# Kernel optimization log

Hardware: AMD Instinct MI355X
Metric: run time of the kernel (lower is better)

## Reference

```python
import jax, jax.numpy as jnp
import numpy as np

K = 3      # kernel size
PAD = 1    # padding
EPS = 1e-5 # BatchNorm eps


def conv3x3(x, w, b):
    out = jax.lax.conv_general_dilated(
        x, w, window_strides=(1, 1), padding=((PAD, PAD), (PAD, PAD)),
        dimension_numbers=('NCHW', 'OIHW', 'NCHW'))
    return out + b[None, :, None, None]


def bilinear_gather(x, py, px):
    # x: [B,C,H,W]; py,px: [B,K2,H,W] fractional sample coords (zero pad OOB)
    B, C, H, W = x.shape
    y0 = jnp.floor(py)
    x0 = jnp.floor(px)
    wy1 = py - y0
    wx1 = px - x0
    xf = x.reshape(B, C, H * W)

    def corner(yc, xc, wgt):
        valid = (yc >= 0) & (yc <= H - 1) & (xc >= 0) & (xc <= W - 1)
        yi = jnp.clip(yc, 0, H - 1).astype(jnp.int32)
        xi = jnp.clip(xc, 0, W - 1).astype(jnp.int32)
        idx = yi * W + xi                      # [B,K2,H,W]
        g = jax.vmap(lambda img, ix: jnp.take(img, ix, axis=1))(xf, idx.reshape(B, -1))
        g = g.reshape(B, C, idx.shape[1], H, W)  # [B,C,K2,H,W]
        return g * (wgt * valid)[:, None]

    return (corner(y0,     x0,     (1 - wy1) * (1 - wx1))
            + corner(y0,     x0 + 1, (1 - wy1) * wx1)
            + corner(y0 + 1, x0,     wy1 * (1 - wx1))
            + corner(y0 + 1, x0 + 1, wy1 * wx1))


def deform_conv_bn_relu(x, offset_w, offset_b, mod_w, mod_b, weight, bias, gamma, beta):
    B, Ci, H, W = x.shape
    Co = weight.shape[0]
    K2 = K * K
    # offset / modulator branches (dense 3x3 convs)
    off = conv3x3(x, offset_w, offset_b)                  # [B,2*K2,H,W]
    mask = 2.0 * jax.nn.sigmoid(conv3x3(x, mod_w, mod_b))  # [B,K2,H,W]
    off = off.reshape(B, K2, 2, H, W)
    dy, dx = off[:, :, 0], off[:, :, 1]
    # base sampling grid per kernel tap
    ii, jj = jnp.meshgrid(jnp.arange(K), jnp.arange(K), indexing='ij')
    ky = ii.reshape(-1).astype(x.dtype)                    # [K2]
    kx = jj.reshape(-1).astype(x.dtype)
    hh = jnp.arange(H, dtype=x.dtype)
    ww = jnp.arange(W, dtype=x.dtype)
    py = hh[None, None, :, None] - PAD + ky[None, :, None, None] + dy  # [B,K2,H,W]
    px = ww[None, None, None, :] - PAD + kx[None, :, None, None] + dx
    sampled = bilinear_gather(x, py, px)                   # [B,Ci,K2,H,W]
    sampled = sampled * mask[:, None]                      # modulated (DCNv2)
    out = jnp.einsum('bckhw,ock->bohw', sampled, weight.reshape(Co, Ci, K2))
    out = out + bias[None, :, None, None]
    # BatchNorm (batch statistics) + ReLU
    mu = out.mean(axis=(0, 2, 3), keepdims=True)
    var = out.var(axis=(0, 2, 3), keepdims=True)
    y = (out - mu) * jax.lax.rsqrt(var + EPS) * gamma[None, :, None, None] + beta[None, :, None, None]
    return jax.nn.relu(y)


def setup_inputs() -> dict:
    key = jax.random.key(0)
    ks = jax.random.split(key, 4)
    B, Ci, Co, H, W = 8, 256, 256, 64, 64
    x = jax.random.normal(ks[0], (B, Ci, H, W), jnp.float32)
    offset_w = jax.random.normal(ks[1], (2 * K * K, Ci, K, K), jnp.float32) * 0.01
    offset_b = jnp.zeros((2 * K * K,), jnp.float32)
    mod_w = jax.random.normal(ks[2], (K * K, Ci, K, K), jnp.float32) * 0.01
    mod_b = jnp.zeros((K * K,), jnp.float32)
    weight = jax.random.normal(ks[3], (Co, Ci, K, K), jnp.float32) * (1.0 / np.sqrt(Ci * K * K))
    bias = jnp.zeros((Co,), jnp.float32)
    gamma = jnp.ones((Co,), jnp.float32)
    beta = jnp.zeros((Co,), jnp.float32)
    return {"x": x, "offset_w": offset_w, "offset_b": offset_b,
            "mod_w": mod_w, "mod_b": mod_b, "weight": weight, "bias": bias,
            "gamma": gamma, "beta": beta}


def reference(x, offset_w, offset_b, mod_w, mod_b, weight, bias, gamma, beta):
    return deform_conv_bn_relu(x, offset_w, offset_b, mod_w, mod_b, weight, bias, gamma, beta)
```

## Files before the change

### kernel.cpp

```cpp
#include <hip/hip_runtime.h>
#include <math.h>

#define CI 256
#define CO 256
#define HWN 4096

typedef short bf16x8 __attribute__((ext_vector_type(8)));
typedef float f32x4 __attribute__((ext_vector_type(4)));

__device__ inline unsigned pk2(float a, float b) {
  unsigned ua = __float_as_uint(a), ub = __float_as_uint(b);
  ua += 0x7fff + ((ua >> 16) & 1);
  ub += 0x7fff + ((ub >> 16) & 1);
  return (ua >> 16) | (ub & 0xffff0000u);
}

#define PIPE_BARRIER()                                    \
  do {                                                    \
    __builtin_amdgcn_sched_barrier(0);                    \
    asm volatile("s_waitcnt lgkmcnt(0)" ::: "memory");    \
    __builtin_amdgcn_s_barrier();                         \
    __builtin_amdgcn_sched_barrier(0);                    \
  } while (0)

__global__ __launch_bounds__(256) void k_prep(
    const float* __restrict__ x, const float* __restrict__ wgt,
    const float* __restrict__ ow, const float* __restrict__ mw,
    unsigned short* __restrict__ wT, unsigned short* __restrict__ wTo,
    unsigned short* __restrict__ xhp) {
  const int bid = blockIdx.x, tid = threadIdx.x;
  if (bid < 4096) {
    int i = bid * 256 + tid;
    const float4* xf = (const float4*)x;
    float4 a = xf[2 * i], b = xf[2 * i + 1];
    ((uint4*)xhp)[i] = make_uint4(pk2(a.x, a.y), pk2(a.z, a.w), pk2(b.x, b.y),
                                  pk2(b.z, b.w));
  } else if (bid < 4352) {
    int o = bid - 4096, c = tid;
    const float* wp = wgt + o * 2304 + c * 9;
    float v[9];
#pragma unroll
    for (int t = 0; t < 9; ++t) v[t] = wp[t];
#pragma unroll
    for (int t = 0; t < 9; ++t) {
      unsigned u = __float_as_uint(v[t]);
      u += 0x7fff + ((u >> 16) & 1);
      wT[(t << 16) + (o << 8) + c] = (unsigned short)(u >> 16);
    }
  } else {
    int o = bid - 4352, c = tid;
    float v[9];
    if (o < 18) {
      const float* wp = ow + o * 2304 + c * 9;
#pragma unroll
      for (int t = 0; t < 9; ++t) v[t] = wp[t];
    } else if (o < 27) {
      const float* wp = mw + (o - 18) * 2304 + c * 9;
#pragma unroll
      for (int t = 0; t < 9; ++t) v[t] = wp[t];
    } else {
#pragma unroll
      for (int t = 0; t < 9; ++t) v[t] = 0.f;
    }
#pragma unroll
    for (int t = 0; t < 9; ++t) {
      unsigned u = __float_as_uint(v[t]);
      u += 0x7fff + ((u >> 16) & 1);
      wTo[(t << 13) + (o << 8) + c] = (unsigned short)(u >> 16);
    }
  }
}

__global__ __launch_bounds__(512, 4) void k_fused2(
    const unsigned short* __restrict__ xh, const unsigned short* __restrict__ wT,
    const unsigned short* __restrict__ wTo, const float* __restrict__ ob,
    const float* __restrict__ mb, float* __restrict__ out,
    float* __restrict__ psum, float* __restrict__ psq) {
  __shared__ __align__(16) char smem[47872];
  uint2* s_cw = (uint2*)smem;
  ushort2* s_ci = (ushort2*)(smem + 4608);
  char* sA = smem + 6912;
  char* sB = smem + 15104;
  float* tr = (float*)(smem + 6912);
  char* sA0 = smem + 6912;
  char* sA1 = smem + 15104;
  char* sB0 = smem + 23296;
  char* sB1 = smem + 27392;
  float* s_red = (float*)(smem + 6912);
  float* s_off = (float*)(smem + 31488);

  const int tid = threadIdx.x;
  const int mblk = blockIdx.x;
  const int b = mblk >> 6, h = mblk & 63;
  const int lane = tid & 63;
  const int wv = tid >> 6;
  const char* xbh = (const char*)(xh + (size_t)b * (CI * HWN));

  {
    const int grp = wv >> 2;
    const int lw = wv & 3;
    const int gtid = tid & 255;
    const int px = lane;
    char* sAg = grp ? sA1 : sA0;
    char* sBg = grp ? sB1 : sB0;
    f32x4 pacc[2];
    pacc[0] = (f32x4){0.f, 0.f, 0.f, 0.f};
    pacc[1] = (f32x4){0.f, 0.f, 0.f, 0.f};

    unsigned rxu[16];
    float cwA, cwB;
    {
      int y0 = h - 1, x0 = px - 1;
      float w = (((unsigned)y0 < 64u) && ((unsigned)x0 < 64u)) ? 1.f : 0.f;
      int y0c = min(max(y0, 0), 63);
      int xp = min(max(x0, 0), 62);
      int s0 = min(max(x0, 0), 63) - xp;
      cwA = s0 ? 0.f : w;
      cwB = s0 ? w : 0.f;
      int ci = y0c * 64 + xp;
#pragma unroll
      for (int g2 = 0; g2 < 2; ++g2) {
        int g = lw + (g2 << 2);
#pragma unroll
        for (int j = 0; j < 8; ++j) {
          int c = ((grp << 1) << 6) + (g << 3) + j;
          __builtin_memcpy(&rxu[(g2 << 3) + j], xbh + (((c << 12) + ci) << 1),
                           4);
        }
      }
    }

#pragma unroll 1
    for (int t = 0; t < 18; ++t) {
      const int cqi = t / 9;
      const int tap = t - cqi * 9;
      const int cq = (grp << 1) + cqi;
#pragma unroll
      for (int g2 = 0; g2 < 2; ++g2) {
        unsigned pkv[4];
#pragma unroll
        for (int j2 = 0; j2 < 4; ++j2) {
          unsigned d0 = rxu[(g2 << 3) + (j2 << 1)];
          unsigned d1 = rxu[(g2 << 3) + (j2 << 1) + 1];
          float v0 = cwA * __uint_as_float(d0 << 16);
          v0 = fmaf(cwB, __uint_as_float(d0 & 0xffff0000u), v0);
          float v1 = cwA * __uint_as_float(d1 << 16);
          v1 = fmaf(cwB, __uint_as_float(d1 & 0xffff0000u), v1);
          pkv[j2] = pk2(v0, v1);
        }
        int g = lw + (g2 << 2);
        *(uint4*)(sAg + (px << 7) + ((g ^ (px & 7)) << 4)) =
            make_uint4(pkv[0], pkv[1], pkv[2], pkv[3]);
      }
      {
        int o = gtid >> 3, seg = gtid & 7;
        uint4 v = *(const uint4*)(wTo + (tap << 13) + (o << 8) + (cq << 6) +
                                  (seg << 3));
        *(uint4*)(sBg + (o << 7) + ((seg ^ (o & 7)) << 4)) = v;
      }
      {
        const int tn = t < 17 ? t + 1 : 17;
        const int cqni = tn / 9;
        const int tapn = tn - cqni * 9;
        const int cqn = (grp << 1) + cqni;
        int ky = tapn / 3, kx = tapn - 3 * ky;
        int y0 = h - 1 + ky, x0 = px - 1 + kx;
        float w = (((unsigned)y0 < 64u) && ((unsigned)x0 < 64u)) ? 1.f : 0.f;
        int y0c = min(max(y0, 0), 63);
        int xp = min(max(x0, 0), 62);
        int s0 = min(max(x0, 0), 63) - xp;
        float cwAn = s0 ? 0.f : w;
        float cwBn = s0 ? w : 0.f;
        int ci = y0c * 64 + xp;
#pragma unroll
        for (int g2 = 0; g2 < 2; ++g2) {
          int g = lw + (g2 << 2);
#pragma unroll
          for (int j = 0; j < 8; ++j) {
            int c = (cqn << 6) + (g << 3) + j;
            __builtin_memcpy(&rxu[(g2 << 3) + j],
                             xbh + (((c << 12) + ci) << 1), 4);
          }
        }
        cwA = cwAn;
        cwB = cwBn;
      }
      PIPE_BARRIER();
#pragma unroll
      for (int ks = 0; ks < 2; ++ks) {
        int arow = (lw << 4) + (lane & 15);
        int aslt = ((ks << 2) + (lane >> 4)) ^ (arow & 7);
        bf16x8 af = *(bf16x8*)(sAg + (arow << 7) + (aslt << 4));
#pragma unroll
        for (int nf = 0; nf < 2; ++nf) {
          int brow = (nf << 4) + (lane & 15);
          int bslt = ((ks << 2) + (lane >> 4)) ^ (brow & 7);
          bf16x8 bfr = *(bf16x8*)(sBg + (brow << 7) + (bslt << 4));
          pacc[nf] = __builtin_amdgcn_mfma_f32_16x16x32_bf16(af, bfr, pacc[nf],
                                                             0, 0, 0);
        }
      }
      PIPE_BARRIER();
    }
    if (grp == 1) {
#pragma unroll
      for (int nf = 0; nf < 2; ++nf)
#pragma unroll
        for (int r = 0; r < 4; ++r) s_red[gtid * 8 + nf * 4 + r] = pacc[nf][r];
    }
    __syncthreads();
    if (grp == 0) {
#pragma unroll
      for (int nf = 0; nf < 2; ++nf) {
#pragma unroll
        for (int r = 0; r < 4; ++r)
          pacc[nf][r] += s_red[gtid * 8 + nf * 4 + r];
        int o = (nf << 4) + (lane & 15);
        int px0 = (lw << 4) + ((lane >> 4) << 2);
        if (o < 18) {
          float bo = ob[o];
          *(float4*)(s_off + o * 64 + px0) =
              make_float4(pacc[nf][0] + bo, pacc[nf][1] + bo, pacc[nf][2] + bo,
                          pacc[nf][3] + bo);
        } else if (o < 27) {
          float bm = mb[o - 18];
          float4 v;
          v.x = 2.f / (1.f + expf(-(pacc[nf][0] + bm)));
          v.y = 2.f / (1.f + expf(-(pacc[nf][1] + bm)));
          v.z = 2.f / (1.f + expf(-(pacc[nf][2] + bm)));
          v.w = 2.f / (1.f + expf(-(pacc[nf][3] + bm)));
          *(float4*)(s_off + o * 64 + px0) = v;
        }
      }
    }
    __syncthreads();
  }

  for (int i = tid; i < 576; i += 512) {
    int k = i >> 6, pxi = i & 63;
    float dy = s_off[(2 * k) * 64 + pxi];
    float dx = s_off[(2 * k + 1) * 64 + pxi];
    float m = s_off[(18 + k) * 64 + pxi];
    float py = (float)(h - 1 + k / 3) + dy;
    float pxf = (float)(pxi - 1 + k % 3) + dx;
    float y0f = floorf(py), x0f = floorf(pxf);
    float wy = py - y0f, wx = pxf - x0f;
    int y0 = (int)y0f, x0 = (int)x0f;
    int y1 = y0 + 1, x1 = x0 + 1;
    float w00 = (1.f - wy) * (1.f - wx) * m;
    float w01 = (1.f - wy) * wx * m;
    float w10 = wy * (1.f - wx) * m;
    float w11 = wy * wx * m;
    bool vy0 = ((unsigned)y0 < 64u), vy1 = ((unsigned)y1 < 64u);
    bool vx0 = ((unsigned)x0 < 64u), vx1 = ((unsigned)x1 < 64u);
    if (!(vy0 && vx0)) w00 = 0.f;
    if (!(vy0 && vx1)) w01 = 0.f;
    if (!(vy1 && vx0)) w10 = 0.f;
    if (!(vy1 && vx1)) w11 = 0.f;
    int y0c = min(max(y0, 0), 63), y1c = min(max(y1, 0), 63);
    int x0c = min(max(x0, 0), 63), x1c = min(max(x1, 0), 63);
    int xp = min(max(x0, 0), 62);
    int s0 = x0c - xp, s1 = x1c - xp;
    float a0 = (s0 ? 0.f : w00) + (s1 ? 0.f : w01);
    float b0 = (s0 ? w00 : 0.f) + (s1 ? w01 : 0.f);
    float a1 = (s0 ? 0.f : w10) + (s1 ? 0.f : w11);
    float b1 = (s0 ? w10 : 0.f) + (s1 ? w11 : 0.f);
    s_cw[i] = make_uint2(pk2(a0, b0), pk2(a1, b1));
    s_ci[i] = make_ushort2((unsigned short)(y0c * 64 + xp),
                           (unsigned short)(y1c * 64 + xp));
  }
  __syncthreads();

  f32x4 acc[4][2];
#pragma unroll
  for (int mf = 0; mf < 4; ++mf)
#pragma unroll
    for (int nf = 0; nf < 2; ++nf) acc[mf][nf] = (f32x4){0.f, 0.f, 0.f, 0.f};

  const int aslot = (lane << 7) + ((wv ^ (lane & 7)) << 4);

  unsigned rxu[16];
  float4 cwC;
  {
    uint2 p = s_cw[lane];
    cwC.x = __uint_as_float(p.x << 16);
    cwC.y = __uint_as_float(p.x & 0xffff0000u);
    cwC.z = __uint_as_float(p.y << 16);
    cwC.w = __uint_as_float(p.y & 0xffff0000u);
    ushort2 ci0 = s_ci[lane];
    const char* xcn = xbh + (((wv << 3) * HWN) << 1);
#pragma unroll
    for (int s = 0; s < 8; ++s) {
      const char* xc = xcn + ((s * HWN) << 1);
      __builtin_memcpy(&rxu[2 * s + 0], xc + ((int)ci0.x << 1), 4);
      __builtin_memcpy(&rxu[2 * s + 1], xc + ((int)ci0.y << 1), 4);
    }
  }

#pragma unroll 1
  for (int t = 0; t < 36; ++t) {
    const int cq = t / 9;
    const int tap = t - cq * 9;
    {
      unsigned pkv[4];
#pragma unroll
      for (int j2 = 0; j2 < 4; ++j2) {
        float vv[2];
#pragma unroll
        for (int u = 0; u < 2; ++u) {
          unsigned d0 = rxu[4 * j2 + 2 * u], d1 = rxu[4 * j2 + 2 * u + 1];
          float v = cwC.x * __uint_as_float(d0 << 16);
          v = fmaf(cwC.y, __uint_as_float(d0 & 0xffff0000u), v);
          v = fmaf(cwC.z, __uint_as_float(d1 << 16), v);
          vv[u] = fmaf(cwC.w, __uint_as_float(d1 & 0xffff0000u), v);
        }
        pkv[j2] = pk2(vv[0], vv[1]);
      }
      *(uint4*)(sA + aslot) = make_uint4(pkv[0], pkv[1], pkv[2], pkv[3]);
    }
    {
      const unsigned short* wp = wT + (tap << 16) + (cq << 6);
#pragma unroll
      for (int r = 0; r < 4; ++r) {
        int idx = (r << 9) + tid;
        int o = idx >> 3, seg = idx & 7;
        uint4 v = *(const uint4*)(wp + (o << 8) + (seg << 3));
        int slot = seg ^ (o & 7);
        *(uint4*)(sB + (o << 7) + (slot << 4)) = v;
      }
    }
    {
      const int tn = t < 35 ? t + 1 : 35;
      const int cqn = tn / 9;
      const int tapn = tn - cqn * 9;
      uint2 p = s_cw[(tapn << 6) + lane];
      float4 cwN;
      cwN.x = __uint_as_float(p.x << 16);
      cwN.y = __uint_as_float(p.x & 0xffff0000u);
      cwN.z = __uint_as_float(p.y << 16);
      cwN.w = __uint_as_float(p.y & 0xffff0000u);
      ushort2 ciN = s_ci[(tapn << 6) + lane];
      const char* xcn = xbh + ((((cqn << 3) + wv) << 3) * HWN << 1);
#pragma unroll
      for (int s = 0; s < 8; ++s) {
        const char* xc = xcn + ((s * HWN) << 1);
        __builtin_memcpy(&rxu[2 * s + 0], xc + ((int)ciN.x << 1), 4);
        __builtin_memcpy(&rxu[2 * s + 1], xc + ((int)ciN.y << 1), 4);
      }
      cwC = cwN;
    }
    PIPE_BARRIER();
#pragma unroll
    for (int ks = 0; ks < 2; ++ks) {
      bf16x8 af[4], bfr[2];
#pragma unroll
      for (int mf = 0; mf < 4; ++mf) {
        int row = (mf << 4) + (lane & 15);
        int slot = ((ks << 2) + (lane >> 4)) ^ (row & 7);
        af[mf] = *(bf16x8*)(sA + (row << 7) + (slot << 4));
      }
#pragma unroll
      for (int nf = 0; nf < 2; ++nf) {
        int row = (wv << 5) + (nf << 4) + (lane & 15);
        int slot = ((ks << 2) + (lane >> 4)) ^ (row & 7);
        bfr[nf] = *(bf16x8*)(sB + (row << 7) + (slot << 4));
      }
#pragma unroll
      for (int mf = 0; mf < 4; ++mf)
#pragma unroll
        for (int nf = 0; nf < 2; ++nf)
          acc[mf][nf] = __builtin_amdgcn_mfma_f32_16x16x32_bf16(
              af[mf], bfr[nf], acc[mf][nf], 0, 0, 0);
    }
    PIPE_BARRIER();
  }

#pragma unroll
  for (int nf = 0; nf < 2; ++nf) {
    float s = 0.f, q = 0.f;
#pragma unroll
    for (int mf = 0; mf < 4; ++mf)
#pragma unroll
      for (int r = 0; r < 4; ++r) {
        float v = acc[mf][nf][r];
        s += v;
        q = fmaf(v, v, q);
      }
    s += __shfl_down(s, 32);
    q += __shfl_down(q, 32);
    s += __shfl_down(s, 16);
    q += __shfl_down(q, 16);
    if (lane < 16) {
      int o = (wv << 5) + (nf << 4) + lane;
      psum[(o << 9) + mblk] = s;
      psq[(o << 9) + mblk] = q;
    }
  }

  __syncthreads();
  for (int p = 0; p < 2; ++p) {
    if ((wv >> 2) == p) {
#pragma unroll
      for (int mf = 0; mf < 4; ++mf)
#pragma unroll
        for (int nf = 0; nf < 2; ++nf) {
          int ro = ((wv & 3) << 5) + (nf << 4) + (lane & 15);
#pragma unroll
          for (int r = 0; r < 4; ++r)
            tr[ro * 65 + (mf << 4) + ((lane >> 4) << 2) + r] = acc[mf][nf][r];
        }
    }
    __syncthreads();
#pragma unroll
    for (int it = 0; it < 4; ++it) {
      int idx = tid + (it << 9);
      int ro = idx >> 4, qd = idx & 15;
      float4 v = make_float4(tr[ro * 65 + qd * 4], tr[ro * 65 + qd * 4 + 1],
                             tr[ro * 65 + qd * 4 + 2], tr[ro * 65 + qd * 4 + 3]);
      *(float4*)(out + (((b << 8) + (p << 7) + ro) << 12) + (h << 6) +
                 (qd << 2)) = v;
    }
    __syncthreads();
  }
}

__global__ __launch_bounds__(256) void k_wprep(const float* __restrict__ wgt,
                                               unsigned short* __restrict__ wT) {
  const int o = blockIdx.x, c = threadIdx.x;
  const float* wp = wgt + o * 2304 + c * 9;
  float v[9];
#pragma unroll
  for (int t = 0; t < 9; ++t) v[t] = wp[t];
#pragma unroll
  for (int t = 0; t < 9; ++t) {
    unsigned u = __float_as_uint(v[t]);
    u += 0x7fff + ((u >> 16) & 1);
    wT[(t << 16) + (o << 8) + c] = (unsigned short)(u >> 16);
  }
}

__global__ __launch_bounds__(512, 4) void k_offmod_fb(
    const float* __restrict__ x, const float* __restrict__ ow,
    const float* __restrict__ ob, const float* __restrict__ mw,
    const float* __restrict__ mb, float* __restrict__ dyb,
    float* __restrict__ dxb, float* __restrict__ mskb) {
  __shared__ float ps[13824];
  const int tid = threadIdx.x;
  const int bid = blockIdx.x;
  const int b = bid & 7;
  const int h = bid >> 3;
  const int cg = __builtin_amdgcn_readfirstlane(tid >> 6);
  const int px = tid & 63;
  float acc[27];
#pragma unroll
  for (int i = 0; i < 27; ++i) acc[i] = 0.f;

  const float* xb = x + b * (CI * HWN);
  const int h0c = max(h - 1, 0), h2c = min(h + 1, 63);
  const bool v0 = h > 0, v2 = h < 63;
  const bool e0 = (px == 0), e63 = (px == 63);
  const float* xw = xb + (cg << 5) * HWN;

#pragma unroll 1
  for (int i = 0; i < 32; ++i) {
    const float* xc = xw + i * HWN;
    float c0 = xc[h0c * 64 + px];
    float c1 = xc[h * 64 + px];
    float c2 = xc[h2c * 64 + px];
    c0 = v0 ? c0 : 0.f;
    c2 = v2 ? c2 : 0.f;
    float l0 = __shfl_up(c0, 1), l1 = __shfl_up(c1, 1), l2 = __shfl_up(c2, 1);
    float r0 = __shfl_down(c0, 1), r1 = __shfl_down(c1, 1),
          r2 = __shfl_down(c2, 1);
    l0 = e0 ? 0.f : l0;
    l1 = e0 ? 0.f : l1;
    l2 = e0 ? 0.f : l2;
    r0 = e63 ? 0.f : r0;
    r1 = e63 ? 0.f : r1;
    r2 = e63 ? 0.f : r2;
    float xv[9] = {l0, c0, r0, l1, c1, r1, l2, c2, r2};
    const int c = (cg << 5) + i;
    const float* owp = ow + c * 9;
    const float* mwp = mw + c * 9;
#pragma unroll
    for (int ch = 0; ch < 18; ++ch)
#pragma unroll
      for (int k = 0; k < 9; ++k)
        acc[ch] = fmaf(owp[ch * 2304 + k], xv[k], acc[ch]);
#pragma unroll
    for (int ch = 0; ch < 9; ++ch)
#pragma unroll
      for (int k = 0; k < 9; ++k)
        acc[18 + ch] = fmaf(mwp[ch * 2304 + k], xv[k], acc[18 + ch]);
  }

#pragma unroll
  for (int ch = 0; ch < 27; ++ch) ps[(px * 27 + ch) * 8 + cg] = acc[ch];
  __syncthreads();
  for (int i = tid; i < 1728; i += 512) {
    int p2 = i / 27;
    int ch = i - p2 * 27;
    float s = 0.f;
#pragma unroll
    for (int g = 0; g < 8; ++g) s += ps[i * 8 + g];
    if (ch < 18) {
      s += ob[ch];
      int k = ch >> 1;
      int o9 = ((b * 9 + k) << 12) + (h << 6) + p2;
      if ((ch & 1) == 0) dyb[o9] = s;
      else dxb[o9] = s;
    } else {
      int k = ch - 18;
      s += mb[k];
      mskb[((b * 9 + k) << 12) + (h << 6) + p2] = 2.f / (1.f + expf(-s));
    }
  }
}

__global__ __launch_bounds__(512, 4) void k_main_f32(
    const float* __restrict__ x, const unsigned short* __restrict__ wT,
    const float* __restrict__ dyb, const float* __restrict__ dxb,
    const float* __restrict__ mskb, float* __restrict__ out,
    float* __restrict__ psum, float* __restrict__ psq) {
  __shared__ __align__(16) char smem[50176];
  uint2* s_cw = (uint2*)smem;
  ushort4* s_ci = (ushort4*)(smem + 4608);
  char* sA = smem + 9216;
  char* sB = smem + 17408;
  float* tr = (float*)(smem + 9216);

  const int tid = threadIdx.x;
  const int mblk = blockIdx.x;
  const int b = mblk >> 6, h = mblk & 63;
  const int lane = tid & 63;
  const int wv = tid >> 6;

  for (int i = tid; i < 576; i += 512) {
    int k = i >> 6, pxi = i & 63;
    int o9 = ((b * 9 + k) << 12) + (h << 6) + pxi;
    float m = mskb[o9];
    float py = (float)(h - 1 + k / 3) + dyb[o9];
    float pxf = (float)(pxi - 1 + k % 3) + dxb[o9];
    float y0f = floorf(py), x0f = floorf(pxf);
    float wy = py - y0f, wx = pxf - x0f;
    int y0 = (int)y0f, x0 = (int)x0f;
    int y1 = y0 + 1, x1 = x0 + 1;
    float w00 = (1.f - wy) * (1.f - wx) * m;
    float w01 = (1.f - wy) * wx * m;
    float w10 = wy * (1.f - wx) * m;
    float w11 = wy * wx * m;
    bool vy0 = ((unsigned)y0 < 64u), vy1 = ((unsigned)y1 < 64u);
    bool vx0 = ((unsigned)x0 < 64u), vx1 = ((unsigned)x1 < 64u);
    if (!(vy0 && vx0)) w00 = 0.f;
    if (!(vy0 && vx1)) w01 = 0.f;
    if (!(vy1 && vx0)) w10 = 0.f;
    if (!(vy1 && vx1)) w11 = 0.f;
    int y0c = min(max(y0, 0), 63), y1c = min(max(y1, 0), 63);
    int x0c = min(max(x0, 0), 63), x1c = min(max(x1, 0), 63);
    s_cw[i] = make_uint2(pk2(w00, w01), pk2(w10, w11));
    s_ci[i] = make_ushort4((unsigned short)(y0c * 64 + x0c),
                           (unsigned short)(y0c * 64 + x1c),
                           (unsigned short)(y1c * 64 + x0c),
                           (unsigned short)(y1c * 64 + x1c));
  }
  __syncthreads();

  f32x4 acc[4][2];
#pragma unroll
  for (int mf = 0; mf < 4; ++mf)
#pragma unroll
    for (int nf = 0; nf < 2; ++nf) acc[mf][nf] = (f32x4){0.f, 0.f, 0.f, 0.f};

  const float* xb = x + b * (CI * HWN);
  const int aslot = (lane << 7) + ((wv ^ (lane & 7)) << 4);

  float rx[32];
  float4 cwC;
  {
    uint2 p = s_cw[lane];
    cwC.x = __uint_as_float(p.x << 16);
    cwC.y = __uint_as_float(p.x & 0xffff0000u);
    cwC.z = __uint_as_float(p.y << 16);
    cwC.w = __uint_as_float(p.y & 0xffff0000u);
    ushort4 ci0 = s_ci[lane];
    const float* xpn = xb + (wv << 3) * HWN;
#pragma unroll
    for (int s = 0; s < 8; ++s) {
      const float* xp = xpn + s * HWN;
      rx[4 * s + 0] = xp[ci0.x];
      rx[4 * s + 1] = xp[ci0.y];
      rx[4 * s + 2] = xp[ci0.z];
      rx[4 * s + 3] = xp[ci0.w];
    }
  }

#pragma unroll 1
  for (int t = 0; t < 36; ++t) {
    const int cq = t / 9;
    const int tap = t - cq * 9;
    {
      unsigned pkv[4];
#pragma unroll
      for (int j2 = 0; j2 < 4; ++j2) {
        float v0 = cwC.x * rx[8 * j2 + 0];
        v0 = fmaf(cwC.y, rx[8 * j2 + 1], v0);
        v0 = fmaf(cwC.z, rx[8 * j2 + 2], v0);
        v0 = fmaf(cwC.w, rx[8 * j2 + 3], v0);
        float v1 = cwC.x * rx[8 * j2 + 4];
        v1 = fmaf(cwC.y, rx[8 * j2 + 5], v1);
        v1 = fmaf(cwC.z, rx[8 * j2 + 6], v1);
        v1 = fmaf(cwC.w, rx[8 * j2 + 7], v1);
        pkv[j2] = pk2(v0, v1);
      }
      *(uint4*)(sA + aslot) = make_uint4(pkv[0], pkv[1], pkv[2], pkv[3]);
    }
    {
      const unsigned short* wp = wT + (tap << 16) + (cq << 6);
#pragma unroll
      for (int r = 0; r < 4; ++r) {
        int idx = (r << 9) + tid;
        int o = idx >> 3, seg = idx & 7;
        uint4 v = *(const uint4*)(wp + (o << 8) + (seg << 3));
        int slot = seg ^ (o & 7);
        *(uint4*)(sB + (o << 7) + (slot << 4)) = v;
      }
    }
    {
      const int tn = t < 35 ? t + 1 : 35;
      const int cqn = tn / 9;
      const int tapn = tn - cqn * 9;
      uint2 p = s_cw[(tapn << 6) + lane];
      float4 cwN;
      cwN.x = __uint_as_float(p.x << 16);
      cwN.y = __uint_as_float(p.x & 0xffff0000u);
      cwN.z = __uint_as_float(p.y << 16);
      cwN.w = __uint_as_float(p.y & 0xffff0000u);
      ushort4 ciN = s_ci[(tapn << 6) + lane];
      const float* xpn = xb + (((cqn << 3) + wv) << 3) * HWN;
#pragma unroll
      for (int s = 0; s < 8; ++s) {
        const float* xp = xpn + s * HWN;
        rx[4 * s + 0] = xp[ciN.x];
        rx[4 * s + 1] = xp[ciN.y];
        rx[4 * s + 2] = xp[ciN.z];
        rx[4 * s + 3] = xp[ciN.w];
      }
      cwC = cwN;
    }
    PIPE_BARRIER();
#pragma unroll
    for (int ks = 0; ks < 2; ++ks) {
      bf16x8 af[4], bfr[2];
#pragma unroll
      for (int mf = 0; mf < 4; ++mf) {
        int row = (mf << 4) + (lane & 15);
        int slot = ((ks << 2) + (lane >> 4)) ^ (row & 7);
        af[mf] = *(bf16x8*)(sA + (row << 7) + (slot << 4));
      }
#pragma unroll
      for (int nf = 0; nf < 2; ++nf) {
        int row = (wv << 5) + (nf << 4) + (lane & 15);
        int slot = ((ks << 2) + (lane >> 4)) ^ (row & 7);
        bfr[nf] = *(bf16x8*)(sB + (row << 7) + (slot << 4));
      }
#pragma unroll
      for (int mf = 0; mf < 4; ++mf)
#pragma unroll
        for (int nf = 0; nf < 2; ++nf)
          acc[mf][nf] = __builtin_amdgcn_mfma_f32_16x16x32_bf16(
              af[mf], bfr[nf], acc[mf][nf], 0, 0, 0);
    }
    PIPE_BARRIER();
  }

#pragma unroll
  for (int nf = 0; nf < 2; ++nf) {
    float s = 0.f, q = 0.f;
#pragma unroll
    for (int mf = 0; mf < 4; ++mf)
#pragma unroll
      for (int r = 0; r < 4; ++r) {
        float v = acc[mf][nf][r];
        s += v;
        q = fmaf(v, v, q);
      }
    s += __shfl_down(s, 32);
    q += __shfl_down(q, 32);
    s += __shfl_down(s, 16);
    q += __shfl_down(q, 16);
    if (lane < 16) {
      int o = (wv << 5) + (nf << 4) + lane;
      psum[(o << 9) + mblk] = s;
      psq[(o << 9) + mblk] = q;
    }
  }

  __syncthreads();
  for (int p = 0; p < 2; ++p) {
    if ((wv >> 2) == p) {
#pragma unroll
      for (int mf = 0; mf < 4; ++mf)
#pragma unroll
        for (int nf = 0; nf < 2; ++nf) {
          int ro = ((wv & 3) << 5) + (nf << 4) + (lane & 15);
#pragma unroll
          for (int r = 0; r < 4; ++r)
            tr[ro * 65 + (mf << 4) + ((lane >> 4) << 2) + r] = acc[mf][nf][r];
        }
    }
    __syncthreads();
#pragma unroll
    for (int it = 0; it < 4; ++it) {
      int idx = tid + (it << 9);
      int ro = idx >> 4, qd = idx & 15;
      float4 v = make_float4(tr[ro * 65 + qd * 4], tr[ro * 65 + qd * 4 + 1],
                             tr[ro * 65 + qd * 4 + 2], tr[ro * 65 + qd * 4 + 3]);
      *(float4*)(out + (((b << 8) + (p << 7) + ro) << 12) + (h << 6) +
                 (qd << 2)) = v;
    }
    __syncthreads();
  }
}

__global__ __launch_bounds__(64) void k_stats(
    const float* __restrict__ psum, const float* __restrict__ psq,
    const float* __restrict__ gamma, const float* __restrict__ beta,
    float* __restrict__ scale, float* __restrict__ shift) {
  const int o = blockIdx.x;
  const int t = threadIdx.x;
  float s = 0.f, q = 0.f;
#pragma unroll
  for (int i = 0; i < 8; ++i) {
    s += psum[(o << 9) + t + (i << 6)];
    q += psq[(o << 9) + t + (i << 6)];
  }
#pragma unroll
  for (int off = 32; off > 0; off >>= 1) {
    s += __shfl_down(s, off, 64);
    q += __shfl_down(q, off, 64);
  }
  if (t == 0) {
    const float inv_n = 1.f / 32768.f;
    float mean = s * inv_n;
    float var = fmaf(-mean, mean, q * inv_n);
    float sc = gamma[o] * rsqrtf(var + 1e-5f);
    scale[o] = sc;
    shift[o] = fmaf(-mean, sc, beta[o]);
  }
}

__global__ __launch_bounds__(256) void k_bnrelu(
    float* __restrict__ out, const float* __restrict__ scale,
    const float* __restrict__ shift) {
  int idx = blockIdx.x * 256 + threadIdx.x;
  int o = (idx >> 10) & 255;
  float sc = scale[o], sh = shift[o];
  float4 v = ((float4*)out)[idx];
  v.x = fmaxf(fmaf(v.x, sc, sh), 0.f);
  v.y = fmaxf(fmaf(v.y, sc, sh), 0.f);
  v.z = fmaxf(fmaf(v.z, sc, sh), 0.f);
  v.w = fmaxf(fmaf(v.w, sc, sh), 0.f);
  ((float4*)out)[idx] = v;
}

extern "C" void kernel_launch(void* const* d_in, const int* in_sizes, int n_in,
                              void* d_out, int out_size, void* d_ws,
                              size_t ws_size, hipStream_t stream) {
  const float* x = (const float*)d_in[0];
  const float* ow = (const float*)d_in[1];
  const float* ob = (const float*)d_in[2];
  const float* mw = (const float*)d_in[3];
  const float* mb = (const float*)d_in[4];
  const float* wgt = (const float*)d_in[5];
  const float* gamma = (const float*)d_in[7];
  const float* beta = (const float*)d_in[8];
  float* out = (float*)d_out;

  float* ws = (float*)d_ws;
  float* dyb = ws;
  float* dxb = dyb + 294912;
  float* mskb = dxb + 294912;
  float* psum = mskb + 294912;
  float* psq = psum + 131072;
  float* scale = psq + 131072;
  float* shift = scale + 256;
  unsigned short* wT = (unsigned short*)(shift + 256);
  unsigned short* xhp = wT + 589824;
  unsigned short* wTo = xhp + 8388608;
  const size_t WS_NEED = (size_t)(294912 * 3 + 131072 * 2 + 512) * 4 +
                         589824 * 2 + 8388608 * 2 + 73728 * 2;

  if (ws_size >= WS_NEED) {
    k_prep<<<4384, 256, 0, stream>>>(x, wgt, ow, mw, wT, wTo, xhp);
    k_fused2<<<512, 512, 0, stream>>>(xhp, wT, wTo, ob, mb, out, psum, psq);
  } else {
    k_wprep<<<256, 256, 0, stream>>>(wgt, wT);
    k_offmod_fb<<<512, 512, 0, stream>>>(x, ow, ob, mw, mb, dyb, dxb, mskb);
    k_main_f32<<<512, 512, 0, stream>>>(x, wT, dyb, dxb, mskb, out, psum, psq);
  }
  k_stats<<<256, 64, 0, stream>>>(psum, psq, gamma, beta, scale, shift);
  k_bnrelu<<<8192, 256, 0, stream>>>(out, scale, shift);
}
```

Measured before the change: 182.6 us.

## Load weight fragments directly to registers and double-buffer A tile with one barrier

The main deformable-conv GEMM loop no longer stages the weight tile through shared memory. Each wave loads its B fragments straight from global memory into registers. The A tile now alternates between two shared buffers, which lets the second barrier per iteration be removed. This cuts LDS traffic and halves the barrier count, at the cost of more global loads per wave, which may be redundant across blocks and are not coalesced into a shared tile, plus extra register pressure.

```diff
diff --git a/kernel.cpp b/kernel.cpp
--- a/kernel.cpp
+++ b/kernel.cpp
@@ -79,11 +79,9 @@
   __shared__ __align__(16) char smem[47872];
   uint2* s_cw = (uint2*)smem;
   ushort2* s_ci = (ushort2*)(smem + 4608);
-  char* sA = smem + 6912;
-  char* sB = smem + 15104;
-  float* tr = (float*)(smem + 6912);
   char* sA0 = smem + 6912;
   char* sA1 = smem + 15104;
+  float* tr = (float*)(smem + 6912);
   char* sB0 = smem + 23296;
   char* sB1 = smem + 27392;
   float* s_red = (float*)(smem + 6912);
@@ -301,6 +299,16 @@
   for (int t = 0; t < 36; ++t) {
     const int cq = t / 9;
     const int tap = t - cq * 9;
+    const unsigned short* wb0 = wT + (tap << 16) +
+                                (((wv << 5) + (lane & 15)) << 8) + (cq << 6) +
+                                ((lane >> 4) << 3);
+    bf16x8 rb[2][2];
+#pragma unroll
+    for (int nf = 0; nf < 2; ++nf)
+#pragma unroll
+      for (int ks = 0; ks < 2; ++ks)
+        rb[nf][ks] = *(const bf16x8*)(wb0 + (nf << 12) + (ks << 5));
+    char* sAw = (t & 1) ? sA1 : sA0;
     {
       unsigned pkv[4];
 #pragma unroll
@@ -316,18 +324,7 @@
         }
         pkv[j2] = pk2(vv[0], vv[1]);
       }
-      *(uint4*)(sA + aslot) = make_uint4(pkv[0], pkv[1], pkv[2], pkv[3]);
-    }
-    {
-      const unsigned short* wp = wT + (tap << 16) + (cq << 6);
-#pragma unroll
-      for (int r = 0; r < 4; ++r) {
-        int idx = (r << 9) + tid;
-        int o = idx >> 3, seg = idx & 7;
-        uint4 v = *(const uint4*)(wp + (o << 8) + (seg << 3));
-        int slot = seg ^ (o & 7);
-        *(uint4*)(sB + (o << 7) + (slot << 4)) = v;
-      }
+      *(uint4*)(sAw + aslot) = make_uint4(pkv[0], pkv[1], pkv[2], pkv[3]);
     }
     {
       const int tn = t < 35 ? t + 1 : 35;
@@ -352,27 +349,20 @@
     PIPE_BARRIER();
 #pragma unroll
     for (int ks = 0; ks < 2; ++ks) {
-      bf16x8 af[4], bfr[2];
+      bf16x8 af[4];
 #pragma unroll
       for (int mf = 0; mf < 4; ++mf) {
         int row = (mf << 4) + (lane & 15);
         int slot = ((ks << 2) + (lane >> 4)) ^ (row & 7);
-        af[mf] = *(bf16x8*)(sA + (row << 7) + (slot << 4));
-      }
-#pragma unroll
-      for (int nf = 0; nf < 2; ++nf) {
-        int row = (wv << 5) + (nf << 4) + (lane & 15);
-        int slot = ((ks << 2) + (lane >> 4)) ^ (row & 7);
-        bfr[nf] = *(bf16x8*)(sB + (row << 7) + (slot << 4));
+        af[mf] = *(bf16x8*)(sAw + (row << 7) + (slot << 4));
       }
 #pragma unroll
       for (int mf = 0; mf < 4; ++mf)
 #pragma unroll
         for (int nf = 0; nf < 2; ++nf)
           acc[mf][nf] = __builtin_amdgcn_mfma_f32_16x16x32_bf16(
-              af[mf], bfr[nf], acc[mf][nf], 0, 0, 0);
-    }
-    PIPE_BARRIER();
+              af[mf], rb[nf][ks], acc[mf][nf], 0, 0, 0);
+    }
   }
 
 #pragma unroll
```

New measurement: 220.2 us. 20.6% more time.
